# Performance work log

Measured on AMD Instinct MI355X. Metric: run time of the kernel, lower is better.

## Reference

```python
import jax, jax.numpy as jnp
import numpy as np

N = 65536        # batch (nodes)
IN_SIZE = 256    # irreps1.dim * irreps2.dim = 16*16
OUT_SIZE = 256
NNZ = 2048       # nonzero Clebsch-Gordan entries


def setup_inputs() -> dict:
    key = jax.random.key(0)
    k1, k2, k3, k4 = jax.random.split(key, 4)
    inp = jax.random.normal(k1, (N, IN_SIZE), dtype=jnp.float32)
    scale = jax.random.normal(k2, (NNZ,), dtype=jnp.float32)
    M_in = jax.random.randint(k3, (NNZ,), 0, IN_SIZE, dtype=jnp.int64)
    M = jnp.sort(jax.random.randint(k4, (NNZ,), 0, OUT_SIZE, dtype=jnp.int64))
    return {"input": inp, "scale": scale, "M_in": M_in, "M": M, "out_size": OUT_SIZE}


def reference(input, scale, M_in, M, out_size):
    # sparse_scale: out[n, M[k]] += scale[k] * input[n, M_in[k]]
    gathered = input[:, M_in] * scale  # [N, nnz]
    # segment-sum over the nnz axis into out_size output slots (M is sorted)
    out = jax.ops.segment_sum(gathered.T, M, num_segments=out_size,
                              indices_are_sorted=True).T  # [N, out_size]
    return out
```

## Files before the change

kernel.cpp:

```cpp
#include <hip/hip_runtime.h>
#include <hip/hip_bf16.h>

#define IN_SZ   256
#define OUT_SZ  256
#define NNZ_C   2048
#define NB      16
#define BMG     64

typedef __attribute__((ext_vector_type(8))) short bf16x8;
typedef __attribute__((ext_vector_type(4))) float f32x4;

static __device__ __forceinline__ short f2bf(float f) {
    __hip_bfloat16 h = __float2bfloat16(f);
    return (short)__builtin_bit_cast(unsigned short, h);
}


__global__ void build_w(const float* __restrict__ scale,
                        const int*   __restrict__ M_in,
                        const int*   __restrict__ M,
                        unsigned short* __restrict__ wb)
{
    __shared__ float row[IN_SZ];
    const int j = blockIdx.x;
    const int t = threadIdx.x;

#pragma unroll
    for (int i = t; i < IN_SZ; i += 64) row[i] = 0.f;
    __syncthreads();

#pragma unroll
    for (int k = t; k < NNZ_C; k += 64)
        if (M[k] == j) atomicAdd(&row[M_in[k]], scale[k]);
    __syncthreads();

    const int wn = j >> 6, n = (j >> 4) & 3, l15 = j & 15;
#pragma unroll
    for (int kk = t; kk < IN_SZ; kk += 64) {
        int kt = kk >> 6, kf = (kk >> 5) & 1, lhi = (kk >> 3) & 3, e = kk & 7;
        int lane = lhi * 16 + l15;
        int c = (((wn * 4 + n) * 4 + kt) * 2 + kf) * 64 + lane;
        wb[c * 8 + e] = (unsigned short)f2bf(row[kk]);
    }
}


__global__ __launch_bounds__(256, 3)
void gemm_direct(const float* __restrict__ input,
                 const bf16x8* __restrict__ wfrag,
                 float* __restrict__ out)
{
    const int tid  = threadIdx.x;
    const int lane = tid & 63;
    const int wn   = tid >> 6;
    const int l15  = lane & 15, lhi = lane >> 4;
    const long row0 = (long)blockIdx.x * BMG;

    f32x4 acc[4][4];
#pragma unroll
    for (int m = 0; m < 4; ++m)
#pragma unroll
        for (int n = 0; n < 4; ++n)
            acc[m][n] = (f32x4){0.f, 0.f, 0.f, 0.f};

#pragma unroll
    for (int kt = 0; kt < 4; ++kt) {
#pragma unroll
        for (int kf = 0; kf < 2; ++kf) {
            bf16x8 afr[4], bfr[4];
#pragma unroll
            for (int m = 0; m < 4; ++m) {
                const float4* p = (const float4*)(input
                    + (row0 + m * 16 + l15) * IN_SZ + kt * 64 + kf * 32 + lhi * 8);
                float4 x = p[0], y = p[1];
                bf16x8 u;
                u[0] = f2bf(x.x); u[1] = f2bf(x.y); u[2] = f2bf(x.z); u[3] = f2bf(x.w);
                u[4] = f2bf(y.x); u[5] = f2bf(y.y); u[6] = f2bf(y.z); u[7] = f2bf(y.w);
                afr[m] = u;
            }
#pragma unroll
            for (int n = 0; n < 4; ++n)
                bfr[n] = wfrag[(((wn * 4 + n) * 4 + kt) * 2 + kf) * 64 + lane];
#pragma unroll
            for (int m = 0; m < 4; ++m)
#pragma unroll
                for (int n = 0; n < 4; ++n)
                    acc[m][n] = __builtin_amdgcn_mfma_f32_16x16x32_bf16(
                        afr[m], bfr[n], acc[m][n], 0, 0, 0);
        }
    }

#pragma unroll
    for (int m = 0; m < 4; ++m) {
        long r0 = row0 + m * 16 + lhi * 4;
#pragma unroll
        for (int n = 0; n < 4; ++n) {
            int col = wn * 64 + n * 16 + l15;
#pragma unroll
            for (int r = 0; r < 4; ++r)
                out[(r0 + r) * OUT_SZ + col] = acc[m][n][r];
        }
    }
}


__global__ __launch_bounds__(256, 4)
void sparse_tp_kernel(const float* __restrict__ input,
                      const float* __restrict__ scale,
                      const int*   __restrict__ M_in,
                      const int*   __restrict__ M,
                      float*       __restrict__ out,
                      int N)
{
    __shared__ float s_in[NB * IN_SZ];
    __shared__ float s_scale[NNZ_C];
    __shared__ int   s_min[NNZ_C];
    __shared__ int   s_seg[OUT_SZ + 1];

    const int tid  = threadIdx.x;
    const int base = blockIdx.x * NB;

    {
        const float4* sc4  = reinterpret_cast<const float4*>(scale);
        const int4*   mi4  = reinterpret_cast<const int4*>(M_in);
        float4*       ssc4 = reinterpret_cast<float4*>(s_scale);
        int4*         smi4 = reinterpret_cast<int4*>(s_min);
        for (int v = tid; v < NNZ_C / 4; v += 256) { ssc4[v] = sc4[v]; smi4[v] = mi4[v]; }
    }
    {
        const float4* in4 = reinterpret_cast<const float4*>(input + (size_t)base * IN_SZ);
        float4*       si4 = reinterpret_cast<float4*>(s_in);
        for (int v = tid; v < NB * IN_SZ / 4; v += 256) {
            int row = v / (IN_SZ / 4);
            if (base + row < N) si4[v] = in4[v];
        }
    }
    {
        int j = tid, lo = 0, hi = NNZ_C;
        while (lo < hi) { int mid = (lo + hi) >> 1; if (M[mid] < j) lo = mid + 1; else hi = mid; }
        s_seg[j] = lo;
        if (tid == 0) s_seg[OUT_SZ] = NNZ_C;
    }
    __syncthreads();

    float acc[NB];
#pragma unroll
    for (int i = 0; i < NB; ++i) acc[i] = 0.f;

    const int j = tid;
    const int k1 = s_seg[j + 1];
    for (int k = s_seg[j]; k < k1; ++k) {
        const float s = s_scale[k];
        const int   m = s_min[k];
#pragma unroll
        for (int i = 0; i < NB; ++i) acc[i] += s * s_in[i * IN_SZ + m];
    }

    float* orow = out + (size_t)base * OUT_SZ + j;
#pragma unroll
    for (int i = 0; i < NB; ++i)
        if (base + i < N) orow[(size_t)i * OUT_SZ] = acc[i];
}


extern "C" void kernel_launch(void* const* d_in, const int* in_sizes, int n_in,
                              void* d_out, int out_size, void* d_ws, size_t ws_size,
                              hipStream_t stream)
{
    const float* input = (const float*)d_in[0];
    const float* scale = (const float*)d_in[1];
    const int*   M_in  = (const int*)d_in[2];
    const int*   M     = (const int*)d_in[3];
    float*       out   = (float*)d_out;

    const int N = in_sizes[0] / IN_SZ;

    if (ws_size >= (size_t)(128 * 1024) && (N % BMG) == 0) {
        unsigned short* wb = (unsigned short*)d_ws;
        build_w    <<<OUT_SZ, 64, 0, stream>>>(scale, M_in, M, wb);
        gemm_direct<<<N / BMG, 256, 0, stream>>>(input, (const bf16x8*)wb, out);
    } else {
        sparse_tp_kernel<<<(N + NB - 1) / NB, 256, 0, stream>>>(input, scale, M_in, M, out, N);
    }
}
```

Before: 157.9 us.

## Stage input tiles through LDS with async double-buffered loads

Replaces the direct per-wave global loads of the input matrix in the GEMM with double-buffered LDS staging via global_load_lds. The buffers use an XOR swizzle to avoid bank conflicts, and the next K-tile of input and weight fragments is prefetched while the current one is computed. Previously all four waves redundantly loaded the same input rows from global memory, and loads were not overlapped with MFMA work. The cost is 32KB of LDS per block, lower occupancy (launch bounds 3 to 2), and barriers each K step.

```diff
diff --git a/kernel.cpp b/kernel.cpp
--- a/kernel.cpp
+++ b/kernel.cpp
@@ -5,7 +5,8 @@
 #define OUT_SZ  256
 #define NNZ_C   2048
 #define NB      16
-#define BMG     64
+#define BM      64
+#define BK      64
 
 typedef __attribute__((ext_vector_type(8))) short bf16x8;
 typedef __attribute__((ext_vector_type(4))) float f32x4;
@@ -45,16 +46,18 @@
 }
 
 
-__global__ __launch_bounds__(256, 3)
-void gemm_direct(const float* __restrict__ input,
+__global__ __launch_bounds__(256, 2)
+void gemm_staged(const float* __restrict__ input,
                  const bf16x8* __restrict__ wfrag,
                  float* __restrict__ out)
 {
+    __shared__ float sA[2][BM * BK];
+
     const int tid  = threadIdx.x;
     const int lane = tid & 63;
-    const int wn   = tid >> 6;
+    const int w    = tid >> 6;
     const int l15  = lane & 15, lhi = lane >> 4;
-    const long row0 = (long)blockIdx.x * BMG;
+    const long row0 = (long)blockIdx.x * BM;
 
     f32x4 acc[4][4];
 #pragma unroll
@@ -63,31 +66,61 @@
         for (int n = 0; n < 4; ++n)
             acc[m][n] = (f32x4){0.f, 0.f, 0.f, 0.f};
 
+    bf16x8 Breg[2][8];
+
+    auto stage = [&](int buf, int kt) {
+#pragma unroll
+        for (int it = 0; it < 4; ++it) {
+            const int c = w * 4 + it;
+            const int r = c * 4 + lhi;
+            const int s = l15 ^ (r & 7);
+            const float* src = input + (row0 + r) * IN_SZ + kt * BK + s * 4;
+            __builtin_amdgcn_global_load_lds(
+                (const __attribute__((address_space(1))) unsigned int*)src,
+                (__attribute__((address_space(3))) unsigned int*)&sA[buf][c * 256],
+                16, 0, 0);
+        }
+    };
+
+    stage(0, 0);
+#pragma unroll
+    for (int i = 0; i < 8; ++i)
+        Breg[0][i] = wfrag[(((w * 4 + (i >> 1)) * 4 + 0) * 2 + (i & 1)) * 64 + lane];
+    __syncthreads();
+
 #pragma unroll
     for (int kt = 0; kt < 4; ++kt) {
+        const int cur = kt & 1;
+        if (kt < 3) {
+#pragma unroll
+            for (int i = 0; i < 8; ++i)
+                Breg[cur ^ 1][i] =
+                    wfrag[(((w * 4 + (i >> 1)) * 4 + (kt + 1)) * 2 + (i & 1)) * 64 + lane];
+            stage(cur ^ 1, kt + 1);
+        }
+
 #pragma unroll
         for (int kf = 0; kf < 2; ++kf) {
-            bf16x8 afr[4], bfr[4];
 #pragma unroll
             for (int m = 0; m < 4; ++m) {
-                const float4* p = (const float4*)(input
-                    + (row0 + m * 16 + l15) * IN_SZ + kt * 64 + kf * 32 + lhi * 8);
-                float4 x = p[0], y = p[1];
+                const int row = m * 16 + l15;
+                const int s0  = kf * 8 + lhi * 2;
+                const int i0  = row * BK + ((s0 ^ (row & 7)) << 2);
+                const int i1  = row * BK + (((s0 + 1) ^ (row & 7)) << 2);
+                f32x4 a0 = *(const f32x4*)&sA[cur][i0];
+                f32x4 a1 = *(const f32x4*)&sA[cur][i1];
                 bf16x8 u;
-                u[0] = f2bf(x.x); u[1] = f2bf(x.y); u[2] = f2bf(x.z); u[3] = f2bf(x.w);
-                u[4] = f2bf(y.x); u[5] = f2bf(y.y); u[6] = f2bf(y.z); u[7] = f2bf(y.w);
-                afr[m] = u;
-            }
-#pragma unroll
-            for (int n = 0; n < 4; ++n)
-                bfr[n] = wfrag[(((wn * 4 + n) * 4 + kt) * 2 + kf) * 64 + lane];
-#pragma unroll
-            for (int m = 0; m < 4; ++m)
+                u[0] = f2bf(a0[0]); u[1] = f2bf(a0[1]);
+                u[2] = f2bf(a0[2]); u[3] = f2bf(a0[3]);
+                u[4] = f2bf(a1[0]); u[5] = f2bf(a1[1]);
+                u[6] = f2bf(a1[2]); u[7] = f2bf(a1[3]);
 #pragma unroll
                 for (int n = 0; n < 4; ++n)
                     acc[m][n] = __builtin_amdgcn_mfma_f32_16x16x32_bf16(
-                        afr[m], bfr[n], acc[m][n], 0, 0, 0);
-        }
+                        u, Breg[cur][n * 2 + kf], acc[m][n], 0, 0, 0);
+            }
+        }
+        __syncthreads();
     }
 
 #pragma unroll
@@ -95,7 +128,7 @@
         long r0 = row0 + m * 16 + lhi * 4;
 #pragma unroll
         for (int n = 0; n < 4; ++n) {
-            int col = wn * 64 + n * 16 + l15;
+            int col = w * 64 + n * 16 + l15;
 #pragma unroll
             for (int r = 0; r < 4; ++r)
                 out[(r0 + r) * OUT_SZ + col] = acc[m][n][r];
@@ -175,10 +208,10 @@
 
     const int N = in_sizes[0] / IN_SZ;
 
-    if (ws_size >= (size_t)(128 * 1024) && (N % BMG) == 0) {
+    if (ws_size >= (size_t)(128 * 1024) && (N % BM) == 0) {
         unsigned short* wb = (unsigned short*)d_ws;
         build_w    <<<OUT_SZ, 64, 0, stream>>>(scale, M_in, M, wb);
-        gemm_direct<<<N / BMG, 256, 0, stream>>>(input, (const bf16x8*)wb, out);
+        gemm_staged<<<N / BM, 256, 0, stream>>>(input, (const bf16x8*)wb, out);
     } else {
         sparse_tp_kernel<<<(N + NB - 1) / NB, 256, 0, stream>>>(input, scale, M_in, M, out, N);
     }
```

Measured after the change: 139.8 us. 11.5% less time.
